# Kernel tuning notes

Hardware: AMD Instinct MI355X
Metric: run time of the kernel (lower is better)

Reference implementation:

```python
import jax, jax.numpy as jnp
import numpy as np

B, S, D = 2, 2048, 2048
RANK = 512
N_HEADS = 16
DROPOUT_RATE = 0.1
KEEP = 1.0 - DROPOUT_RATE  # original safe_dropout scales by 1/keep even when deterministic


def setup_inputs() -> dict:
    key = jax.random.key(0)
    ks = jax.random.split(key, 9)
    return {
        "x": jax.random.normal(ks[0], (B, S, D), jnp.float32),
        "g_Q": jax.random.uniform(ks[1], (B, S, RANK), jnp.float32),
        "g_K": jax.random.uniform(ks[2], (B, S, RANK), jnp.float32),
        "g_V": jax.random.uniform(ks[3], (B, S, RANK), jnp.float32),
        "qk_read": jax.random.normal(ks[4], (RANK, D), jnp.float32) * 0.02,
        "qk_write": jax.random.normal(ks[5], (RANK, D), jnp.float32) * 0.02,
        "v_read": jax.random.normal(ks[6], (RANK, D), jnp.float32) * 0.02,
        "v_write": jax.random.normal(ks[7], (RANK, D), jnp.float32) * 0.02,
        "W_O": jax.random.normal(ks[8], (D, D), jnp.float32) * 0.02,
    }


def _gated_lowrank(x, g, rd, wr):
    # g * (x @ rd.T) @ wr : [B,S,D] -> [B,S,rank] -> [B,S,D]
    return (g * jnp.einsum('bsd,rd->bsr', x, rd)) @ wr


def reference(x, g_Q, g_K, g_V, qk_read, qk_write, v_read, v_write, W_O):
    Bx, Sx, Dx = x.shape
    d_head = Dx // N_HEADS

    Q = _gated_lowrank(x, g_Q, qk_read, qk_write)
    K = _gated_lowrank(x, g_K, qk_read, qk_write)
    V = _gated_lowrank(x, g_V, v_read, v_write)

    Q = Q.reshape(Bx, Sx, N_HEADS, d_head).transpose(0, 2, 1, 3)
    K = K.reshape(Bx, Sx, N_HEADS, d_head).transpose(0, 2, 1, 3)
    V = V.reshape(Bx, Sx, N_HEADS, d_head).transpose(0, 2, 1, 3)

    scale = jnp.sqrt(jnp.float32(d_head))
    scores = jnp.einsum('bhsd,bhtd->bhst', Q, K) / scale  # [B,H,S,S]
    causal = jnp.tril(jnp.ones((Sx, Sx), dtype=jnp.bool_))
    scores = jnp.where(causal, scores, jnp.finfo(scores.dtype).min)
    attn_w = jax.nn.softmax(scores, axis=-1)
    attn_w = attn_w / KEEP  # deterministic branch of original safe_dropout

    out = jnp.einsum('bhst,bhtd->bhsd', attn_w, V)
    out = out.transpose(0, 2, 1, 3).reshape(Bx, Sx, Dx)
    out = out @ W_O
    out = out / KEEP  # deterministic dropout scaling
    return out
```

## Files before the change

### kernel.cpp

```cpp
#include <hip/hip_runtime.h>
#include <cstdint>
#include <cstddef>

typedef unsigned short u16;
typedef unsigned int u32;
typedef __attribute__((ext_vector_type(4))) float f32x4;
typedef __attribute__((ext_vector_type(8))) __bf16 bf16x8;
typedef __attribute__((ext_vector_type(8))) u16 u16x8;
typedef __attribute__((ext_vector_type(4))) u16 u16x4;
typedef __attribute__((ext_vector_type(2))) u32 u32x2;

__device__ __forceinline__ u16 f2bf(float x) {
  u32 u = __builtin_bit_cast(u32, x);
  u += 0x7fffu + ((u >> 16) & 1u);
  return (u16)(u >> 16);
}
__device__ __forceinline__ float bf2f(u16 b) {
  return __builtin_bit_cast(float, (u32)b << 16);
}
__device__ __forceinline__ bf16x8 ldfrag(const u16* p) {
  return __builtin_bit_cast(bf16x8, *(const u16x8*)p);
}
__device__ __forceinline__ void gload_lds16(const void* g, void* l) {
  auto gp = (const __attribute__((address_space(1))) u32*)g;
  auto lp = (__attribute__((address_space(3))) u32*)l;
  __builtin_amdgcn_global_load_lds(gp, lp, 16, 0, 0);
}
#define MFMA16(a, b, c) __builtin_amdgcn_mfma_f32_16x16x32_bf16(a, b, c, 0, 0, 0)


__global__ void cvt_kernel(const float* __restrict__ in, u16* __restrict__ out, int n) {
  int i = (blockIdx.x * blockDim.x + threadIdx.x) * 4;
  if (i >= n) return;
  f32x4 v = *(const f32x4*)(in + i);
  u16x4 r = { f2bf(v[0]), f2bf(v[1]), f2bf(v[2]), f2bf(v[3]) };
  *(u16x4*)(out + i) = r;
}

__global__ void tcvt_kernel(const float* __restrict__ in, u16* __restrict__ out, int R, int C) {
  __shared__ float tile[32][33];
  int bx = blockIdx.x * 32, by = blockIdx.y * 32;
  int tx = threadIdx.x, ty = threadIdx.y;
#pragma unroll
  for (int i = 0; i < 32; i += 8)
    tile[ty + i][tx] = in[(size_t)(by + ty + i) * C + bx + tx];
  __syncthreads();
#pragma unroll
  for (int i = 0; i < 32; i += 8)
    out[(size_t)(bx + ty + i) * R + by + tx] = f2bf(tile[tx][ty + i]);
}

__global__ void gate_kernel(const float* __restrict__ gq, const float* __restrict__ gk,
                            const float* __restrict__ gv, const u16* __restrict__ Pcat,
                            u16* __restrict__ Aq, u16* __restrict__ Ak, u16* __restrict__ Av,
                            int n) {
  const float SC = 0.1275255128608411f;
  int i = (blockIdx.x * blockDim.x + threadIdx.x) * 4;
  if (i >= n) return;
  int s = i >> 9;
  int r = i & 511;
  u16x4 pq = *(const u16x4*)(Pcat + (size_t)s * 1024 + r);
  u16x4 pv = *(const u16x4*)(Pcat + (size_t)s * 1024 + 512 + r);
  f32x4 q = *(const f32x4*)(gq + i);
  f32x4 k = *(const f32x4*)(gk + i);
  f32x4 v = *(const f32x4*)(gv + i);
  u16x4 aq, ak, av;
#pragma unroll
  for (int j = 0; j < 4; ++j) {
    float pf = bf2f(pq[j]);
    float vf = bf2f(pv[j]);
    aq[j] = f2bf(q[j] * SC * pf);
    ak[j] = f2bf(k[j] * pf);
    av[j] = f2bf(v[j] * vf);
  }
  *(u16x4*)(Aq + i) = aq;
  *(u16x4*)(Ak + i) = ak;
  *(u16x4*)(Av + i) = av;
}

template <bool F32OUT>
__global__ void gemm_bt(const u16* __restrict__ A, const u16* __restrict__ Bt,
                        void* __restrict__ Cp, int M, int N, int K, float scale) {
  __shared__ u16 Al[128 * 32];
  __shared__ u16 Bl[128 * 32];
  const int tid = threadIdx.x;
  const int lane = tid & 63;
  const int w = tid >> 6;
  const int wr = (w >> 1) * 64;
  const int wc = (w & 1) * 64;
  const size_t bm = (size_t)blockIdx.y * 128;
  const size_t bn = (size_t)blockIdx.x * 128;

  f32x4 acc[4][4] = {};

  const int srow = lane >> 2;
  const int sch = lane & 3;
  const int kc = lane >> 4;
  const int rl = lane & 15;

  for (int kt = 0; kt < K; kt += 32) {
#pragma unroll
    for (int half = 0; half < 2; ++half) {
      int rb = half * 64 + w * 16;
      int row = rb + srow;
      int ch = sch ^ ((row >> 1) & 3);
      gload_lds16(A + (bm + row) * (size_t)K + kt + ch * 8, &Al[rb * 32]);
    }
#pragma unroll
    for (int half = 0; half < 2; ++half) {
      int rb = half * 64 + w * 16;
      int row = rb + srow;
      int ch = sch ^ ((row >> 1) & 3);
      gload_lds16(Bt + (bn + row) * (size_t)K + kt + ch * 8, &Bl[rb * 32]);
    }
    asm volatile("s_waitcnt vmcnt(0)" ::: "memory");
    __syncthreads();

    bf16x8 af[4], bfr[4];
#pragma unroll
    for (int m = 0; m < 4; ++m) {
      int row = wr + m * 16 + rl;
      af[m] = ldfrag(&Al[row * 32 + (kc ^ ((row >> 1) & 3)) * 8]);
    }
#pragma unroll
    for (int n = 0; n < 4; ++n) {
      int row = wc + n * 16 + rl;
      bfr[n] = ldfrag(&Bl[row * 32 + (kc ^ ((row >> 1) & 3)) * 8]);
    }
#pragma unroll
    for (int m = 0; m < 4; ++m)
#pragma unroll
      for (int n = 0; n < 4; ++n)
        acc[m][n] = MFMA16(af[m], bfr[n], acc[m][n]);
    __syncthreads();
  }

  const int r0 = (lane >> 4) * 4;
#pragma unroll
  for (int m = 0; m < 4; ++m) {
    size_t grow = bm + wr + m * 16 + r0;
#pragma unroll
    for (int n = 0; n < 4; ++n) {
      size_t gcol = bn + wc + n * 16 + rl;
#pragma unroll
      for (int r = 0; r < 4; ++r) {
        float v = acc[m][n][r] * scale;
        if constexpr (F32OUT)
          ((float*)Cp)[(grow + r) * (size_t)N + gcol] = v;
        else
          ((u16*)Cp)[(grow + r) * (size_t)N + gcol] = f2bf(v);
      }
    }
  }
}

__global__ __launch_bounds__(256, 3) void attn_kernel(const u16* __restrict__ Q,
                                                      const u16* __restrict__ Kg,
                                                      const u16* __restrict__ Vt,
                                                      u16* __restrict__ AO) {
  __shared__ u16 Kl[2][64 * 128];
  __shared__ u16 Vl[128 * 64];

  const int tid = threadIdx.x;
  const int lane = tid & 63;
  const int w = tid >> 6;
  const int bh = blockIdx.x;
  const int qb = 31 - blockIdx.y;
  const int b = bh >> 4;
  const int h = bh & 15;

  const int rl = lane & 15;
  const int g4 = lane >> 4;

  const float THR = 10.0f;

  bf16x8 ones;
  {
    u16x8 ou;
#pragma unroll
    for (int j = 0; j < 8; ++j) ou[j] = 0x3F80;
    ones = __builtin_bit_cast(bf16x8, ou);
  }

  auto stageK = [&](int buf, int t0) {
    int roff = lane >> 4;
    int cch = lane & 15;
#pragma unroll
    for (int i = 0; i < 4; ++i) {
      int rb = w * 16 + i * 4;
      int row = rb + roff;
      int ch = cch ^ (row & 7);
      gload_lds16(Kg + ((size_t)b * 2048 + t0 + row) * 2048 + h * 128 + ch * 8,
                  &Kl[buf][rb * 128]);
    }
  };
  auto stageV = [&](int t0) {
    int roff = lane >> 3;
    int cch = lane & 7;
#pragma unroll
    for (int i = 0; i < 4; ++i) {
      int rb = w * 32 + i * 8;
      int row = rb + roff;
      int ch = cch ^ (row & 7);
      gload_lds16(Vt + (size_t)(h * 128 + row) * 4096 + (size_t)b * 2048 + t0 + ch * 8,
                  &Vl[rb * 64]);
    }
  };

  const int ntiles = qb + 1;
  const int qq = qb * 64 + w * 16 + rl;
  const size_t qrow0 = (size_t)b * 2048 + (size_t)qb * 64;

  bf16x8 qf[4];
  {
    const u16* qp = Q + (qrow0 + w * 16 + rl) * 2048 + h * 128 + g4 * 8;
#pragma unroll
    for (int ks = 0; ks < 4; ++ks) qf[ks] = ldfrag(qp + ks * 32);
  }

  float m_r = -3.0e38f;
  float l_r[4];
#pragma unroll
  for (int r = 0; r < 4; ++r) l_r[r] = 0.f;
  f32x4 oacc[8] = {};

  stageK(0, 0);
  __syncthreads();
  int cur = 0;

#pragma unroll 1
  for (int t = 0; t < ntiles; ++t) {
    const int t0 = t * 64;
    stageV(t0);
    const bool pref = (t + 1 < ntiles);
    if (pref) stageK(cur ^ 1, (t + 1) * 64);

    float p[4][4];
    __builtin_amdgcn_s_setprio(1);
#pragma unroll
    for (int nf = 0; nf < 4; ++nf) {
      f32x4 c = {};
      int trow = nf * 16 + rl;
#pragma unroll
      for (int ks = 0; ks < 4; ++ks) {
        bf16x8 kf = ldfrag(&Kl[cur][trow * 128 + ((ks * 4 + g4) ^ (trow & 7)) * 8]);
        c = MFMA16(kf, qf[ks], c);
      }
      if (t == qb) {
        int tb = t0 + nf * 16 + g4 * 4;
#pragma unroll
        for (int r = 0; r < 4; ++r)
          p[nf][r] = (tb + r <= qq) ? c[r] : -3.0e38f;
      } else {
#pragma unroll
        for (int r = 0; r < 4; ++r) p[nf][r] = c[r];
      }
    }
    __builtin_amdgcn_s_setprio(0);

    float mx = p[0][0];
#pragma unroll
    for (int nf = 0; nf < 4; ++nf)
#pragma unroll
      for (int r = 0; r < 4; ++r) mx = fmaxf(mx, p[nf][r]);
    mx = fmaxf(mx, __shfl_xor(mx, 16));
    mx = fmaxf(mx, __shfl_xor(mx, 32));

    if (__any(mx - m_r > THR)) {
      float mn = fmaxf(m_r, mx);
      float alpha = exp2f(m_r - mn);
      m_r = mn;
#pragma unroll
      for (int r = 0; r < 4; ++r) {
        float av = __shfl(alpha, g4 * 4 + r, 16);
        l_r[r] *= av;
#pragma unroll
        for (int nf = 0; nf < 8; ++nf) oacc[nf][r] *= av;
      }
    }

    u32x2 pk[4];
#pragma unroll
    for (int nf = 0; nf < 4; ++nf) {
      u32 e0 = __builtin_bit_cast(u32, exp2f(p[nf][0] - m_r));
      u32 e1 = __builtin_bit_cast(u32, exp2f(p[nf][1] - m_r));
      u32 e2 = __builtin_bit_cast(u32, exp2f(p[nf][2] - m_r));
      u32 e3 = __builtin_bit_cast(u32, exp2f(p[nf][3] - m_r));
      pk[nf][0] = (e1 & 0xffff0000u) | (e0 >> 16);
      pk[nf][1] = (e3 & 0xffff0000u) | (e2 >> 16);
    }

    if (pref) asm volatile("s_waitcnt vmcnt(4)\n\ts_barrier" ::: "memory");
    else      asm volatile("s_waitcnt vmcnt(0)\n\ts_barrier" ::: "memory");

    u16* pl = &Kl[cur][w * 1024];
#pragma unroll
    for (int nf = 0; nf < 4; ++nf) {
      int c8 = ((nf * 2 + (g4 >> 1)) ^ (rl & 7)) * 8 + (g4 & 1) * 4;
      *(u32x2*)(&pl[rl * 64 + c8]) = pk[nf];
    }

    __builtin_amdgcn_s_setprio(1);
    f32x4 rs = {};
#pragma unroll
    for (int ks = 0; ks < 2; ++ks) {
      bf16x8 pa = ldfrag(&pl[rl * 64 + ((ks * 4 + g4) ^ (rl & 7)) * 8]);
#pragma unroll
      for (int nf = 0; nf < 8; ++nf) {
        int drow = nf * 16 + rl;
        bf16x8 vf = ldfrag(&Vl[drow * 64 + ((ks * 4 + g4) ^ (drow & 7)) * 8]);
        oacc[nf] = MFMA16(pa, vf, oacc[nf]);
      }
      rs = MFMA16(pa, ones, rs);
    }
    __builtin_amdgcn_s_setprio(0);
#pragma unroll
    for (int r = 0; r < 4; ++r) l_r[r] += rs[r];

    __syncthreads();
    cur ^= 1;
  }

#pragma unroll
  for (int nf = 0; nf < 8; ++nf) {
    size_t dc = (size_t)h * 128 + nf * 16 + rl;
#pragma unroll
    for (int r = 0; r < 4; ++r) {
      float v = oacc[nf][r] / l_r[r];
      AO[(qrow0 + w * 16 + g4 * 4 + r) * 2048 + dc] = f2bf(v);
    }
  }
}


extern "C" void kernel_launch(void* const* d_in, const int* in_sizes, int n_in,
                              void* d_out, int out_size, void* d_ws, size_t ws_size,
                              hipStream_t stream) {
  const float* x = (const float*)d_in[0];
  const float* gQ = (const float*)d_in[1];
  const float* gK = (const float*)d_in[2];
  const float* gV = (const float*)d_in[3];
  const float* qkr = (const float*)d_in[4];
  const float* qkw = (const float*)d_in[5];
  const float* vr = (const float*)d_in[6];
  const float* vw = (const float*)d_in[7];
  const float* wo = (const float*)d_in[8];
  float* out = (float*)d_out;

  u16* p = (u16*)d_ws;
  u16* x_bf = p;   p += 8388608;
  u16* qkr_b = p;  p += 1048576;
  u16* vr_b = p;   p += 1048576;
  u16* qkwT = p;   p += 1048576;
  u16* vwT = p;    p += 1048576;
  u16* woT = p;    p += 4194304;
  u16* Pcat = p;   p += 4194304;
  u16* Aq = p;     p += 2097152;
  u16* Ak = p;     p += 2097152;
  u16* Av = p;     p += 2097152;
  u16* Qb = p;     p += 8388608;
  u16* Kb = p;     p += 8388608;
  u16* Vt = x_bf;
  u16* AO = Qb;

  cvt_kernel<<<8192, 256, 0, stream>>>(x, x_bf, 8388608);
  cvt_kernel<<<1024, 256, 0, stream>>>(qkr, qkr_b, 1048576);
  cvt_kernel<<<1024, 256, 0, stream>>>(vr, vr_b, 1048576);
  tcvt_kernel<<<dim3(64, 16), dim3(32, 8), 0, stream>>>(qkw, qkwT, 512, 2048);
  tcvt_kernel<<<dim3(64, 16), dim3(32, 8), 0, stream>>>(vw, vwT, 512, 2048);
  tcvt_kernel<<<dim3(64, 64), dim3(32, 8), 0, stream>>>(wo, woT, 2048, 2048);

  gemm_bt<false><<<dim3(8, 32), 256, 0, stream>>>(x_bf, qkr_b, Pcat, 4096, 1024, 2048, 1.f);

  gate_kernel<<<2048, 256, 0, stream>>>(gQ, gK, gV, Pcat, Aq, Ak, Av, 2097152);

  gemm_bt<false><<<dim3(16, 64), 256, 0, stream>>>(Aq, qkwT, Qb, 8192, 2048, 512, 1.f);

  gemm_bt<false><<<dim3(32, 16), 256, 0, stream>>>(vwT, Av, Vt, 2048, 4096, 512, 1.f);

  attn_kernel<<<dim3(32, 32), 256, 0, stream>>>(Qb, Kb, Vt, AO);

  gemm_bt<true><<<dim3(16, 32), 256, 0, stream>>>(AO, woT, out, 4096, 2048, 2048,
                                                  1.2345679012345678f);
}
```

Baseline: 227.2 us.

## Fuse gating into projection GEMM and double query rows per attention block

Folds the gate multiply into the epilogue of the x-by-read-weight GEMM, so the intermediate Pcat buffer and the separate gate kernel are dropped. The attention kernel now handles 128 query rows per block (two 16-row groups per wave), so each staged K/V tile is reused twice as much, and the grid is halved. Occupancy drops to 2 blocks per CU from register pressure, and waves whose rows lie below the current key tile skip compute while still taking part in barriers. The fused epilogue uses scalar, less coalesced stores and gate loads.

```diff
diff --git a/kernel.cpp b/kernel.cpp
--- a/kernel.cpp
+++ b/kernel.cpp
@@ -48,34 +48,6 @@
 #pragma unroll
   for (int i = 0; i < 32; i += 8)
     out[(size_t)(bx + ty + i) * R + by + tx] = f2bf(tile[tx][ty + i]);
-}
-
-__global__ void gate_kernel(const float* __restrict__ gq, const float* __restrict__ gk,
-                            const float* __restrict__ gv, const u16* __restrict__ Pcat,
-                            u16* __restrict__ Aq, u16* __restrict__ Ak, u16* __restrict__ Av,
-                            int n) {
-  const float SC = 0.1275255128608411f;
-  int i = (blockIdx.x * blockDim.x + threadIdx.x) * 4;
-  if (i >= n) return;
-  int s = i >> 9;
-  int r = i & 511;
-  u16x4 pq = *(const u16x4*)(Pcat + (size_t)s * 1024 + r);
-  u16x4 pv = *(const u16x4*)(Pcat + (size_t)s * 1024 + 512 + r);
-  f32x4 q = *(const f32x4*)(gq + i);
-  f32x4 k = *(const f32x4*)(gk + i);
-  f32x4 v = *(const f32x4*)(gv + i);
-  u16x4 aq, ak, av;
-#pragma unroll
-  for (int j = 0; j < 4; ++j) {
-    float pf = bf2f(pq[j]);
-    float vf = bf2f(pv[j]);
-    aq[j] = f2bf(q[j] * SC * pf);
-    ak[j] = f2bf(k[j] * pf);
-    av[j] = f2bf(v[j] * vf);
-  }
-  *(u16x4*)(Aq + i) = aq;
-  *(u16x4*)(Ak + i) = ak;
-  *(u16x4*)(Av + i) = av;
 }
 
 template <bool F32OUT>
@@ -154,7 +126,90 @@
   }
 }
 
-__global__ __launch_bounds__(256, 3) void attn_kernel(const u16* __restrict__ Q,
+__global__ void gemm_gate(const u16* __restrict__ A, const u16* __restrict__ Bt,
+                          const float* __restrict__ gq, const float* __restrict__ gk,
+                          const float* __restrict__ gv, u16* __restrict__ Aq,
+                          u16* __restrict__ Ak, u16* __restrict__ Av, int K) {
+  __shared__ u16 Al[128 * 32];
+  __shared__ u16 Bl[128 * 32];
+  const float SC = 0.1275255128608411f;
+  const int tid = threadIdx.x;
+  const int lane = tid & 63;
+  const int w = tid >> 6;
+  const int wr = (w >> 1) * 64;
+  const int wc = (w & 1) * 64;
+  const size_t bm = (size_t)blockIdx.y * 128;
+  const size_t bn = (size_t)blockIdx.x * 128;
+
+  f32x4 acc[4][4] = {};
+
+  const int srow = lane >> 2;
+  const int sch = lane & 3;
+  const int kc = lane >> 4;
+  const int rl = lane & 15;
+
+  for (int kt = 0; kt < K; kt += 32) {
+#pragma unroll
+    for (int half = 0; half < 2; ++half) {
+      int rb = half * 64 + w * 16;
+      int row = rb + srow;
+      int ch = sch ^ ((row >> 1) & 3);
+      gload_lds16(A + (bm + row) * (size_t)K + kt + ch * 8, &Al[rb * 32]);
+    }
+#pragma unroll
+    for (int half = 0; half < 2; ++half) {
+      int rb = half * 64 + w * 16;
+      int row = rb + srow;
+      int ch = sch ^ ((row >> 1) & 3);
+      gload_lds16(Bt + (bn + row) * (size_t)K + kt + ch * 8, &Bl[rb * 32]);
+    }
+    asm volatile("s_waitcnt vmcnt(0)" ::: "memory");
+    __syncthreads();
+
+    bf16x8 af[4], bfr[4];
+#pragma unroll
+    for (int m = 0; m < 4; ++m) {
+      int row = wr + m * 16 + rl;
+      af[m] = ldfrag(&Al[row * 32 + (kc ^ ((row >> 1) & 3)) * 8]);
+    }
+#pragma unroll
+    for (int n = 0; n < 4; ++n) {
+      int row = wc + n * 16 + rl;
+      bfr[n] = ldfrag(&Bl[row * 32 + (kc ^ ((row >> 1) & 3)) * 8]);
+    }
+#pragma unroll
+    for (int m = 0; m < 4; ++m)
+#pragma unroll
+      for (int n = 0; n < 4; ++n)
+        acc[m][n] = MFMA16(af[m], bfr[n], acc[m][n]);
+    __syncthreads();
+  }
+
+  const int r0 = (lane >> 4) * 4;
+  const bool phalf = (bn < 512);
+#pragma unroll
+  for (int m = 0; m < 4; ++m) {
+    size_t grow = bm + wr + m * 16 + r0;
+#pragma unroll
+    for (int n = 0; n < 4; ++n) {
+      size_t gcol = bn + wc + n * 16 + rl;
+#pragma unroll
+      for (int r = 0; r < 4; ++r) {
+        float v = acc[m][n][r];
+        if (phalf) {
+          size_t idx = (grow + r) * 512 + gcol;
+          Aq[idx] = f2bf(gq[idx] * SC * v);
+          Ak[idx] = f2bf(gk[idx] * v);
+        } else {
+          size_t idx = (grow + r) * 512 + (gcol - 512);
+          Av[idx] = f2bf(gv[idx] * v);
+        }
+      }
+    }
+  }
+}
+
+__global__ __launch_bounds__(256, 2) void attn_kernel(const u16* __restrict__ Q,
                                                       const u16* __restrict__ Kg,
                                                       const u16* __restrict__ Vt,
                                                       u16* __restrict__ AO) {
@@ -165,7 +220,7 @@
   const int lane = tid & 63;
   const int w = tid >> 6;
   const int bh = blockIdx.x;
-  const int qb = 31 - blockIdx.y;
+  const int qb = 15 - blockIdx.y;
   const int b = bh >> 4;
   const int h = bh & 15;
 
@@ -207,22 +262,29 @@
     }
   };
 
-  const int ntiles = qb + 1;
-  const int qq = qb * 64 + w * 16 + rl;
-  const size_t qrow0 = (size_t)b * 2048 + (size_t)qb * 64;
-
-  bf16x8 qf[4];
+  const int ntiles = 2 * qb + 2;
+  const int qhb0 = qb * 128 + w * 32;
+  const int qq0 = qhb0 + rl;
+  const int qq1 = qhb0 + 16 + rl;
+  const int qmax = qhb0 + 31;
+  const size_t qrow0 = (size_t)b * 2048 + (size_t)qb * 128;
+
+  bf16x8 qf0[4], qf1[4];
   {
-    const u16* qp = Q + (qrow0 + w * 16 + rl) * 2048 + h * 128 + g4 * 8;
-#pragma unroll
-    for (int ks = 0; ks < 4; ++ks) qf[ks] = ldfrag(qp + ks * 32);
-  }
-
-  float m_r = -3.0e38f;
-  float l_r[4];
-#pragma unroll
-  for (int r = 0; r < 4; ++r) l_r[r] = 0.f;
-  f32x4 oacc[8] = {};
+    const u16* qp0 = Q + (qrow0 + w * 32 + rl) * 2048 + h * 128 + g4 * 8;
+    const u16* qp1 = qp0 + 16 * 2048;
+#pragma unroll
+    for (int ks = 0; ks < 4; ++ks) {
+      qf0[ks] = ldfrag(qp0 + ks * 32);
+      qf1[ks] = ldfrag(qp1 + ks * 32);
+    }
+  }
+
+  float m_r0 = -3.0e38f, m_r1 = -3.0e38f;
+  float l_r0[4], l_r1[4];
+#pragma unroll
+  for (int r = 0; r < 4; ++r) { l_r0[r] = 0.f; l_r1[r] = 0.f; }
+  f32x4 oacc0[8] = {}, oacc1[8] = {};
 
   stageK(0, 0);
   __syncthreads();
@@ -235,87 +297,114 @@
     const bool pref = (t + 1 < ntiles);
     if (pref) stageK(cur ^ 1, (t + 1) * 64);
 
-    float p[4][4];
-    __builtin_amdgcn_s_setprio(1);
-#pragma unroll
-    for (int nf = 0; nf < 4; ++nf) {
-      f32x4 c = {};
-      int trow = nf * 16 + rl;
-#pragma unroll
-      for (int ks = 0; ks < 4; ++ks) {
-        bf16x8 kf = ldfrag(&Kl[cur][trow * 128 + ((ks * 4 + g4) ^ (trow & 7)) * 8]);
-        c = MFMA16(kf, qf[ks], c);
-      }
-      if (t == qb) {
+    if (t0 <= qmax) {
+      float p0[4][4], p1[4][4];
+      const bool nm0 = (t0 + 63 > qhb0);
+      const bool nm1 = (t0 + 63 > qhb0 + 16);
+      __builtin_amdgcn_s_setprio(1);
+#pragma unroll
+      for (int nf = 0; nf < 4; ++nf) {
+        f32x4 c0 = {}, c1 = {};
+        int trow = nf * 16 + rl;
+#pragma unroll
+        for (int ks = 0; ks < 4; ++ks) {
+          bf16x8 kf = ldfrag(&Kl[cur][trow * 128 + ((ks * 4 + g4) ^ (trow & 7)) * 8]);
+          c0 = MFMA16(kf, qf0[ks], c0);
+          c1 = MFMA16(kf, qf1[ks], c1);
+        }
         int tb = t0 + nf * 16 + g4 * 4;
-#pragma unroll
-        for (int r = 0; r < 4; ++r)
-          p[nf][r] = (tb + r <= qq) ? c[r] : -3.0e38f;
-      } else {
-#pragma unroll
-        for (int r = 0; r < 4; ++r) p[nf][r] = c[r];
-      }
-    }
-    __builtin_amdgcn_s_setprio(0);
-
-    float mx = p[0][0];
-#pragma unroll
-    for (int nf = 0; nf < 4; ++nf)
-#pragma unroll
-      for (int r = 0; r < 4; ++r) mx = fmaxf(mx, p[nf][r]);
-    mx = fmaxf(mx, __shfl_xor(mx, 16));
-    mx = fmaxf(mx, __shfl_xor(mx, 32));
-
-    if (__any(mx - m_r > THR)) {
-      float mn = fmaxf(m_r, mx);
-      float alpha = exp2f(m_r - mn);
-      m_r = mn;
-#pragma unroll
-      for (int r = 0; r < 4; ++r) {
-        float av = __shfl(alpha, g4 * 4 + r, 16);
-        l_r[r] *= av;
-#pragma unroll
-        for (int nf = 0; nf < 8; ++nf) oacc[nf][r] *= av;
-      }
-    }
-
-    u32x2 pk[4];
-#pragma unroll
-    for (int nf = 0; nf < 4; ++nf) {
-      u32 e0 = __builtin_bit_cast(u32, exp2f(p[nf][0] - m_r));
-      u32 e1 = __builtin_bit_cast(u32, exp2f(p[nf][1] - m_r));
-      u32 e2 = __builtin_bit_cast(u32, exp2f(p[nf][2] - m_r));
-      u32 e3 = __builtin_bit_cast(u32, exp2f(p[nf][3] - m_r));
-      pk[nf][0] = (e1 & 0xffff0000u) | (e0 >> 16);
-      pk[nf][1] = (e3 & 0xffff0000u) | (e2 >> 16);
-    }
-
-    if (pref) asm volatile("s_waitcnt vmcnt(4)\n\ts_barrier" ::: "memory");
-    else      asm volatile("s_waitcnt vmcnt(0)\n\ts_barrier" ::: "memory");
-
-    u16* pl = &Kl[cur][w * 1024];
-#pragma unroll
-    for (int nf = 0; nf < 4; ++nf) {
-      int c8 = ((nf * 2 + (g4 >> 1)) ^ (rl & 7)) * 8 + (g4 & 1) * 4;
-      *(u32x2*)(&pl[rl * 64 + c8]) = pk[nf];
-    }
-
-    __builtin_amdgcn_s_setprio(1);
-    f32x4 rs = {};
-#pragma unroll
-    for (int ks = 0; ks < 2; ++ks) {
-      bf16x8 pa = ldfrag(&pl[rl * 64 + ((ks * 4 + g4) ^ (rl & 7)) * 8]);
-#pragma unroll
-      for (int nf = 0; nf < 8; ++nf) {
-        int drow = nf * 16 + rl;
-        bf16x8 vf = ldfrag(&Vl[drow * 64 + ((ks * 4 + g4) ^ (drow & 7)) * 8]);
-        oacc[nf] = MFMA16(pa, vf, oacc[nf]);
-      }
-      rs = MFMA16(pa, ones, rs);
-    }
-    __builtin_amdgcn_s_setprio(0);
-#pragma unroll
-    for (int r = 0; r < 4; ++r) l_r[r] += rs[r];
+        if (nm0) {
+#pragma unroll
+          for (int r = 0; r < 4; ++r) p0[nf][r] = (tb + r <= qq0) ? c0[r] : -3.0e38f;
+        } else {
+#pragma unroll
+          for (int r = 0; r < 4; ++r) p0[nf][r] = c0[r];
+        }
+        if (nm1) {
+#pragma unroll
+          for (int r = 0; r < 4; ++r) p1[nf][r] = (tb + r <= qq1) ? c1[r] : -3.0e38f;
+        } else {
+#pragma unroll
+          for (int r = 0; r < 4; ++r) p1[nf][r] = c1[r];
+        }
+      }
+      __builtin_amdgcn_s_setprio(0);
+
+      float mx0 = p0[0][0], mx1 = p1[0][0];
+#pragma unroll
+      for (int nf = 0; nf < 4; ++nf)
+#pragma unroll
+        for (int r = 0; r < 4; ++r) {
+          mx0 = fmaxf(mx0, p0[nf][r]);
+          mx1 = fmaxf(mx1, p1[nf][r]);
+        }
+      mx0 = fmaxf(mx0, __shfl_xor(mx0, 16));
+      mx0 = fmaxf(mx0, __shfl_xor(mx0, 32));
+      mx1 = fmaxf(mx1, __shfl_xor(mx1, 16));
+      mx1 = fmaxf(mx1, __shfl_xor(mx1, 32));
+
+      if (__any(fmaxf(mx0 - m_r0, mx1 - m_r1) > THR)) {
+        float mn0 = fmaxf(m_r0, mx0), mn1 = fmaxf(m_r1, mx1);
+        float a0 = exp2f(m_r0 - mn0), a1 = exp2f(m_r1 - mn1);
+        m_r0 = mn0; m_r1 = mn1;
+#pragma unroll
+        for (int r = 0; r < 4; ++r) {
+          float av0 = __shfl(a0, g4 * 4 + r, 16);
+          float av1 = __shfl(a1, g4 * 4 + r, 16);
+          l_r0[r] *= av0; l_r1[r] *= av1;
+#pragma unroll
+          for (int nf = 0; nf < 8; ++nf) { oacc0[nf][r] *= av0; oacc1[nf][r] *= av1; }
+        }
+      }
+
+      u32x2 pk0[4], pk1[4];
+#pragma unroll
+      for (int nf = 0; nf < 4; ++nf) {
+        u32 e0 = __builtin_bit_cast(u32, exp2f(p0[nf][0] - m_r0));
+        u32 e1 = __builtin_bit_cast(u32, exp2f(p0[nf][1] - m_r0));
+        u32 e2 = __builtin_bit_cast(u32, exp2f(p0[nf][2] - m_r0));
+        u32 e3 = __builtin_bit_cast(u32, exp2f(p0[nf][3] - m_r0));
+        pk0[nf][0] = (e1 & 0xffff0000u) | (e0 >> 16);
+        pk0[nf][1] = (e3 & 0xffff0000u) | (e2 >> 16);
+        u32 f0 = __builtin_bit_cast(u32, exp2f(p1[nf][0] - m_r1));
+        u32 f1 = __builtin_bit_cast(u32, exp2f(p1[nf][1] - m_r1));
+        u32 f2 = __builtin_bit_cast(u32, exp2f(p1[nf][2] - m_r1));
+        u32 f3 = __builtin_bit_cast(u32, exp2f(p1[nf][3] - m_r1));
+        pk1[nf][0] = (f1 & 0xffff0000u) | (f0 >> 16);
+        pk1[nf][1] = (f3 & 0xffff0000u) | (f2 >> 16);
+      }
+
+      if (pref) asm volatile("s_waitcnt vmcnt(4)\n\ts_barrier" ::: "memory");
+      else      asm volatile("s_waitcnt vmcnt(0)\n\ts_barrier" ::: "memory");
+
+      u16* pl = &Kl[cur][w * 2048];
+#pragma unroll
+      for (int nf = 0; nf < 4; ++nf) {
+        int c8 = ((nf * 2 + (g4 >> 1)) ^ (rl & 7)) * 8 + (g4 & 1) * 4;
+        *(u32x2*)(&pl[rl * 64 + c8]) = pk0[nf];
+        *(u32x2*)(&pl[(16 + rl) * 64 + c8]) = pk1[nf];
+      }
+
+      __builtin_amdgcn_s_setprio(1);
+      f32x4 rs0 = {}, rs1 = {};
+#pragma unroll
+      for (int ks = 0; ks < 2; ++ks) {
+        bf16x8 pa0 = ldfrag(&pl[rl * 64 + ((ks * 4 + g4) ^ (rl & 7)) * 8]);
+        bf16x8 pa1 = ldfrag(&pl[(16 + rl) * 64 + ((ks * 4 + g4) ^ (rl & 7)) * 8]);
+#pragma unroll
+        for (int nf = 0; nf < 8; ++nf) {
+          int drow = nf * 16 + rl;
+          bf16x8 vf = ldfrag(&Vl[drow * 64 + ((ks * 4 + g4) ^ (drow & 7)) * 8]);
+          oacc0[nf] = MFMA16(pa0, vf, oacc0[nf]);
+          oacc1[nf] = MFMA16(pa1, vf, oacc1[nf]);
+        }
+        rs0 = MFMA16(pa0, ones, rs0);
+        rs1 = MFMA16(pa1, ones, rs1);
+      }
+      __builtin_amdgcn_s_setprio(0);
+#pragma unroll
+      for (int r = 0; r < 4; ++r) { l_r0[r] += rs0[r]; l_r1[r] += rs1[r]; }
+    }
 
     __syncthreads();
     cur ^= 1;
@@ -326,8 +415,8 @@
     size_t dc = (size_t)h * 128 + nf * 16 + rl;
 #pragma unroll
     for (int r = 0; r < 4; ++r) {
-      float v = oacc[nf][r] / l_r[r];
-      AO[(qrow0 + w * 16 + g4 * 4 + r) * 2048 + dc] = f2bf(v);
+      AO[(qrow0 + w * 32 + g4 * 4 + r) * 2048 + dc] = f2bf(oacc0[nf][r] / l_r0[r]);
+      AO[(qrow0 + w * 32 + 16 + g4 * 4 + r) * 2048 + dc] = f2bf(oacc1[nf][r] / l_r1[r]);
     }
   }
 }
@@ -354,7 +443,6 @@
   u16* qkwT = p;   p += 1048576;
   u16* vwT = p;    p += 1048576;
   u16* woT = p;    p += 4194304;
-  u16* Pcat = p;   p += 4194304;
   u16* Aq = p;     p += 2097152;
   u16* Ak = p;     p += 2097152;
   u16* Av = p;     p += 2097152;
@@ -370,15 +458,13 @@
   tcvt_kernel<<<dim3(64, 16), dim3(32, 8), 0, stream>>>(vw, vwT, 512, 2048);
   tcvt_kernel<<<dim3(64, 64), dim3(32, 8), 0, stream>>>(wo, woT, 2048, 2048);
 
-  gemm_bt<false><<<dim3(8, 32), 256, 0, stream>>>(x_bf, qkr_b, Pcat, 4096, 1024, 2048, 1.f);
-
-  gate_kernel<<<2048, 256, 0, stream>>>(gQ, gK, gV, Pcat, Aq, Ak, Av, 2097152);
+  gemm_gate<<<dim3(8, 32), 256, 0, stream>>>(x_bf, qkr_b, gQ, gK, gV, Aq, Ak, Av, 2048);
 
   gemm_bt<false><<<dim3(16, 64), 256, 0, stream>>>(Aq, qkwT, Qb, 8192, 2048, 512, 1.f);
 
   gemm_bt<false><<<dim3(32, 16), 256, 0, stream>>>(vwT, Av, Vt, 2048, 4096, 512, 1.f);
 
-  attn_kernel<<<dim3(32, 32), 256, 0, stream>>>(Qb, Kb, Vt, AO);
+  attn_kernel<<<dim3(32, 16), 256, 0, stream>>>(Qb, Kb, Vt, AO);
 
   gemm_bt<true><<<dim3(16, 32), 256, 0, stream>>>(AO, woT, out, 4096, 2048, 2048,
                                                   1.2345679012345678f);
```

Result: slower. 257.1 us (+13.2%).

## Fuse gating into projection GEMM epilogue and merge prep and QKV launches

Applied to the files above, without the earlier changes.

Combines all fp32-to-bf16 conversion and transpose kernels into a single launch. Applies the gating multiply directly in the epilogue of the x-projection GEMM, eliminating the intermediate Pcat buffer and the separate gate kernel. Runs the Q/K and V projection GEMMs in one launch. This cuts launch overhead and intermediate memory traffic, but the epilogue now does uncoalesced scalar loads of the gate tensors.

```diff
diff --git a/kernel.cpp b/kernel.cpp
--- a/kernel.cpp
+++ b/kernel.cpp
@@ -28,61 +28,152 @@
 }
 #define MFMA16(a, b, c) __builtin_amdgcn_mfma_f32_16x16x32_bf16(a, b, c, 0, 0, 0)
 
-
-__global__ void cvt_kernel(const float* __restrict__ in, u16* __restrict__ out, int n) {
-  int i = (blockIdx.x * blockDim.x + threadIdx.x) * 4;
-  if (i >= n) return;
-  f32x4 v = *(const f32x4*)(in + i);
-  u16x4 r = { f2bf(v[0]), f2bf(v[1]), f2bf(v[2]), f2bf(v[3]) };
-  *(u16x4*)(out + i) = r;
-}
-
-__global__ void tcvt_kernel(const float* __restrict__ in, u16* __restrict__ out, int R, int C) {
+__global__ void prep_kernel(const float* __restrict__ x, const float* __restrict__ qkr,
+                            const float* __restrict__ vr, const float* __restrict__ qkw,
+                            const float* __restrict__ vw, const float* __restrict__ wo,
+                            u16* __restrict__ x_bf, u16* __restrict__ qkr_b,
+                            u16* __restrict__ vr_b, u16* __restrict__ qkwT,
+                            u16* __restrict__ vwT, u16* __restrict__ woT) {
   __shared__ float tile[32][33];
-  int bx = blockIdx.x * 32, by = blockIdx.y * 32;
-  int tx = threadIdx.x, ty = threadIdx.y;
-#pragma unroll
-  for (int i = 0; i < 32; i += 8)
-    tile[ty + i][tx] = in[(size_t)(by + ty + i) * C + bx + tx];
-  __syncthreads();
-#pragma unroll
-  for (int i = 0; i < 32; i += 8)
-    out[(size_t)(bx + ty + i) * R + by + tx] = f2bf(tile[tx][ty + i]);
-}
-
-__global__ void gate_kernel(const float* __restrict__ gq, const float* __restrict__ gk,
-                            const float* __restrict__ gv, const u16* __restrict__ Pcat,
-                            u16* __restrict__ Aq, u16* __restrict__ Ak, u16* __restrict__ Av,
-                            int n) {
-  const float SC = 0.1275255128608411f;
-  int i = (blockIdx.x * blockDim.x + threadIdx.x) * 4;
-  if (i >= n) return;
-  int s = i >> 9;
-  int r = i & 511;
-  u16x4 pq = *(const u16x4*)(Pcat + (size_t)s * 1024 + r);
-  u16x4 pv = *(const u16x4*)(Pcat + (size_t)s * 1024 + 512 + r);
-  f32x4 q = *(const f32x4*)(gq + i);
-  f32x4 k = *(const f32x4*)(gk + i);
-  f32x4 v = *(const f32x4*)(gv + i);
-  u16x4 aq, ak, av;
-#pragma unroll
-  for (int j = 0; j < 4; ++j) {
-    float pf = bf2f(pq[j]);
-    float vf = bf2f(pv[j]);
-    aq[j] = f2bf(q[j] * SC * pf);
-    ak[j] = f2bf(k[j] * pf);
-    av[j] = f2bf(v[j] * vf);
-  }
-  *(u16x4*)(Aq + i) = aq;
-  *(u16x4*)(Ak + i) = ak;
-  *(u16x4*)(Av + i) = av;
+  const int bid = blockIdx.x;
+  const int tid = threadIdx.x;
+  if (bid < 10240) {
+    const float* in;
+    u16* out;
+    int base;
+    if (bid < 8192) { in = x; out = x_bf; base = bid; }
+    else if (bid < 9216) { in = qkr; out = qkr_b; base = bid - 8192; }
+    else { in = vr; out = vr_b; base = bid - 9216; }
+    int i = base * 1024 + tid * 4;
+    f32x4 v = *(const f32x4*)(in + i);
+    u16x4 r = { f2bf(v[0]), f2bf(v[1]), f2bf(v[2]), f2bf(v[3]) };
+    *(u16x4*)(out + i) = r;
+  } else {
+    const float* in;
+    u16* out;
+    int R, C, local;
+    if (bid < 11264) { in = qkw; out = qkwT; R = 512; C = 2048; local = bid - 10240; }
+    else if (bid < 12288) { in = vw; out = vwT; R = 512; C = 2048; local = bid - 11264; }
+    else { in = wo; out = woT; R = 2048; C = 2048; local = bid - 12288; }
+    int bx = (local & 63) * 32, by = (local >> 6) * 32;
+    int tx = tid & 31, ty = tid >> 5;
+#pragma unroll
+    for (int i = 0; i < 32; i += 8)
+      tile[ty + i][tx] = in[(size_t)(by + ty + i) * C + bx + tx];
+    __syncthreads();
+#pragma unroll
+    for (int i = 0; i < 32; i += 8)
+      out[(size_t)(bx + ty + i) * R + by + tx] = f2bf(tile[tx][ty + i]);
+  }
+}
+
+template <bool F32OUT>
+__device__ __forceinline__ void gemm_body(const u16* __restrict__ A,
+                                          const u16* __restrict__ Bt,
+                                          void* __restrict__ Cp, int N, int K,
+                                          float scale, size_t bm, size_t bn,
+                                          u16* Al, u16* Bl) {
+  const int tid = threadIdx.x;
+  const int lane = tid & 63;
+  const int w = tid >> 6;
+  const int wr = (w >> 1) * 64;
+  const int wc = (w & 1) * 64;
+
+  f32x4 acc[4][4] = {};
+
+  const int srow = lane >> 2;
+  const int sch = lane & 3;
+  const int kc = lane >> 4;
+  const int rl = lane & 15;
+
+  for (int kt = 0; kt < K; kt += 32) {
+#pragma unroll
+    for (int half = 0; half < 2; ++half) {
+      int rb = half * 64 + w * 16;
+      int row = rb + srow;
+      int ch = sch ^ ((row >> 1) & 3);
+      gload_lds16(A + (bm + row) * (size_t)K + kt + ch * 8, &Al[rb * 32]);
+    }
+#pragma unroll
+    for (int half = 0; half < 2; ++half) {
+      int rb = half * 64 + w * 16;
+      int row = rb + srow;
+      int ch = sch ^ ((row >> 1) & 3);
+      gload_lds16(Bt + (bn + row) * (size_t)K + kt + ch * 8, &Bl[rb * 32]);
+    }
+    asm volatile("s_waitcnt vmcnt(0)" ::: "memory");
+    __syncthreads();
+
+    bf16x8 af[4], bfr[4];
+#pragma unroll
+    for (int m = 0; m < 4; ++m) {
+      int row = wr + m * 16 + rl;
+      af[m] = ldfrag(&Al[row * 32 + (kc ^ ((row >> 1) & 3)) * 8]);
+    }
+#pragma unroll
+    for (int n = 0; n < 4; ++n) {
+      int row = wc + n * 16 + rl;
+      bfr[n] = ldfrag(&Bl[row * 32 + (kc ^ ((row >> 1) & 3)) * 8]);
+    }
+#pragma unroll
+    for (int m = 0; m < 4; ++m)
+#pragma unroll
+      for (int n = 0; n < 4; ++n)
+        acc[m][n] = MFMA16(af[m], bfr[n], acc[m][n]);
+    __syncthreads();
+  }
+
+  const int r0 = (lane >> 4) * 4;
+#pragma unroll
+  for (int m = 0; m < 4; ++m) {
+    size_t grow = bm + wr + m * 16 + r0;
+#pragma unroll
+    for (int n = 0; n < 4; ++n) {
+      size_t gcol = bn + wc + n * 16 + rl;
+#pragma unroll
+      for (int r = 0; r < 4; ++r) {
+        float v = acc[m][n][r] * scale;
+        if constexpr (F32OUT)
+          ((float*)Cp)[(grow + r) * (size_t)N + gcol] = v;
+        else
+          ((u16*)Cp)[(grow + r) * (size_t)N + gcol] = f2bf(v);
+      }
+    }
+  }
 }
 
 template <bool F32OUT>
 __global__ void gemm_bt(const u16* __restrict__ A, const u16* __restrict__ Bt,
-                        void* __restrict__ Cp, int M, int N, int K, float scale) {
+                        void* __restrict__ Cp, int N, int K, float scale) {
   __shared__ u16 Al[128 * 32];
   __shared__ u16 Bl[128 * 32];
+  gemm_body<F32OUT>(A, Bt, Cp, N, K, scale, (size_t)blockIdx.y * 128,
+                    (size_t)blockIdx.x * 128, Al, Bl);
+}
+
+__global__ void gemm_qkv(const u16* __restrict__ Acat, const u16* __restrict__ qkwT,
+                         u16* __restrict__ Qb, const u16* __restrict__ vwT,
+                         const u16* __restrict__ Av, u16* __restrict__ Vt) {
+  __shared__ u16 Al[128 * 32];
+  __shared__ u16 Bl[128 * 32];
+  const int bid = blockIdx.x;
+  if (bid < 1024) {
+    gemm_body<false>(Acat, qkwT, Qb, 2048, 512, 1.f, (size_t)(bid >> 4) * 128,
+                     (size_t)(bid & 15) * 128, Al, Bl);
+  } else {
+    const int l = bid - 1024;
+    gemm_body<false>(vwT, Av, Vt, 4096, 512, 1.f, (size_t)(l >> 5) * 128,
+                     (size_t)(l & 31) * 128, Al, Bl);
+  }
+}
+
+__global__ void gemm_gate(const u16* __restrict__ A, const u16* __restrict__ Bt,
+                          const float* __restrict__ gq, const float* __restrict__ gk,
+                          const float* __restrict__ gv, u16* __restrict__ Aq,
+                          u16* __restrict__ Ak, u16* __restrict__ Av, int K) {
+  __shared__ u16 Al[128 * 32];
+  __shared__ u16 Bl[128 * 32];
+  const float SC = 0.1275255128608411f;
   const int tid = threadIdx.x;
   const int lane = tid & 63;
   const int w = tid >> 6;
@@ -136,6 +227,7 @@
   }
 
   const int r0 = (lane >> 4) * 4;
+  const bool phalf = (bn < 512);
 #pragma unroll
   for (int m = 0; m < 4; ++m) {
     size_t grow = bm + wr + m * 16 + r0;
@@ -144,11 +236,15 @@
       size_t gcol = bn + wc + n * 16 + rl;
 #pragma unroll
       for (int r = 0; r < 4; ++r) {
-        float v = acc[m][n][r] * scale;
-        if constexpr (F32OUT)
-          ((float*)Cp)[(grow + r) * (size_t)N + gcol] = v;
-        else
-          ((u16*)Cp)[(grow + r) * (size_t)N + gcol] = f2bf(v);
+        float v = acc[m][n][r];
+        if (phalf) {
+          size_t idx = (grow + r) * 512 + gcol;
+          Aq[idx] = f2bf(gq[idx] * SC * v);
+          Ak[idx] = f2bf(gk[idx] * v);
+        } else {
+          size_t idx = (grow + r) * 512 + (gcol - 512);
+          Av[idx] = f2bf(gv[idx] * v);
+        }
       }
     }
   }
@@ -354,7 +450,6 @@
   u16* qkwT = p;   p += 1048576;
   u16* vwT = p;    p += 1048576;
   u16* woT = p;    p += 4194304;
-  u16* Pcat = p;   p += 4194304;
   u16* Aq = p;     p += 2097152;
   u16* Ak = p;     p += 2097152;
   u16* Av = p;     p += 2097152;
@@ -363,23 +458,15 @@
   u16* Vt = x_bf;
   u16* AO = Qb;
 
-  cvt_kernel<<<8192, 256, 0, stream>>>(x, x_bf, 8388608);
-  cvt_kernel<<<1024, 256, 0, stream>>>(qkr, qkr_b, 1048576);
-  cvt_kernel<<<1024, 256, 0, stream>>>(vr, vr_b, 1048576);
-  tcvt_kernel<<<dim3(64, 16), dim3(32, 8), 0, stream>>>(qkw, qkwT, 512, 2048);
-  tcvt_kernel<<<dim3(64, 16), dim3(32, 8), 0, stream>>>(vw, vwT, 512, 2048);
-  tcvt_kernel<<<dim3(64, 64), dim3(32, 8), 0, stream>>>(wo, woT, 2048, 2048);
-
-  gemm_bt<false><<<dim3(8, 32), 256, 0, stream>>>(x_bf, qkr_b, Pcat, 4096, 1024, 2048, 1.f);
-
-  gate_kernel<<<2048, 256, 0, stream>>>(gQ, gK, gV, Pcat, Aq, Ak, Av, 2097152);
-
-  gemm_bt<false><<<dim3(16, 64), 256, 0, stream>>>(Aq, qkwT, Qb, 8192, 2048, 512, 1.f);
-
-  gemm_bt<false><<<dim3(32, 16), 256, 0, stream>>>(vwT, Av, Vt, 2048, 4096, 512, 1.f);
+  prep_kernel<<<16384, 256, 0, stream>>>(x, qkr, vr, qkw, vw, wo,
+                                         x_bf, qkr_b, vr_b, qkwT, vwT, woT);
+
+  gemm_gate<<<dim3(8, 32), 256, 0, stream>>>(x_bf, qkr_b, gQ, gK, gV, Aq, Ak, Av, 2048);
+
+  gemm_qkv<<<1536, 256, 0, stream>>>(Aq, qkwT, Qb, vwT, Av, Vt);
 
   attn_kernel<<<dim3(32, 32), 256, 0, stream>>>(Qb, Kb, Vt, AO);
 
-  gemm_bt<true><<<dim3(16, 32), 256, 0, stream>>>(AO, woT, out, 4096, 2048, 2048,
+  gemm_bt<true><<<dim3(16, 32), 256, 0, stream>>>(AO, woT, out, 2048, 2048,
                                                   1.2345679012345678f);
 }
```

Result: faster. 221.9 us (-2.4%).
